# Kernel tuning notes

Hardware: AMD Instinct MI355X
Metric: run time of the kernel (lower is better)

Reference implementation:

```python
import math
import jax, jax.numpy as jnp
from jax import lax
import numpy as np

N = 512          # transform size; frame size = 2N
B = 16           # batch
T = 2048         # number of frames; signal length = N*T
PI = math.pi


def _make_mdct_filter(n: int, normalize: bool = True) -> jnp.ndarray:
    # filter[k, 0, t] = cos(pi/N * (t + 0.5 + N/2) * (k + 0.5)) / sqrt(N)
    k = jnp.arange(n, dtype=jnp.float32).reshape(n, 1, 1)
    t = jnp.arange(2 * n, dtype=jnp.float32).reshape(1, 1, 2 * n)
    f = jnp.cos(PI / n * (t + 0.5 + n / 2) * (k + 0.5))
    if normalize:
        f = f / jnp.sqrt(jnp.float32(n))
    return f  # [N, 1, 2N]


def setup_inputs() -> dict:
    key = jax.random.key(0)
    x = jax.random.normal(key, (B, 1, N * T), dtype=jnp.float32)
    mdct_filter = _make_mdct_filter(N, normalize=True)
    return {"x": x, "mdct_filter": mdct_filter}


def reference(x, mdct_filter):
    # Equivalent of F.conv1d(x, filter, stride=N, padding=N)
    n = mdct_filter.shape[0]
    # x: [B, 1, N*T] -> out: [B, N, T+1]
    out = lax.conv_general_dilated(
        x, mdct_filter,
        window_strides=(n,),
        padding=[(n, n)],
        dimension_numbers=("NCH", "OIH", "NCH"),
    )
    return out
```

## Files before the change

### kernel.cpp

```cpp
#include <hip/hip_runtime.h>
#include <hip/hip_bf16.h>
#include <stdint.h>
#include <stddef.h>


constexpr int N_ = 512;
constexpr int T_ = 2048;
constexpr int B_ = 16;
constexpr int LEN = N_ * T_;
constexpr int FRAMES = T_ + 1;
constexpr int COLS = B_ * FRAMES;
constexpr int NT_TILES = 257;
constexpr int COLS_PAD = NT_TILES * 128;
constexpr int KF = 512;
constexpr int BK = 64;

typedef __attribute__((ext_vector_type(8))) _Float16 f16x8;
typedef __attribute__((ext_vector_type(4))) _Float16 f16x4;
typedef __attribute__((ext_vector_type(4))) float f32x4;

#define GLD16(gptr, lptr)                                                     \
  __builtin_amdgcn_global_load_lds(                                           \
      (const __attribute__((address_space(1))) unsigned int*)(gptr),          \
      (__attribute__((address_space(3))) unsigned int*)(lptr), 16, 0, 0)

__global__ void prep_filter(const float* __restrict__ f,
                            _Float16* __restrict__ D) {
  int idx = (blockIdx.x * 256 + threadIdx.x) * 4;
  int k = idx >> 9;
  int j = idx & 511;
  int t = (j < 256) ? j : (j + 256);
  const float4 v = *(const float4*)&f[k * 1024 + t];
  f16x4 h = {(_Float16)v.x, (_Float16)v.y, (_Float16)v.z, (_Float16)v.w};
  *(f16x4*)&D[k * KF + j] = h;
}

__global__ void fold_x(const float* __restrict__ x, _Float16* __restrict__ V) {
  const int c = blockIdx.x * 4 + (threadIdx.x >> 6);
  const int l = threadIdx.x & 63;
  const bool mi = (l < 32);
  const int j0 = mi ? (l * 8) : (256 + (l - 32) * 8);
  const float sgn = mi ? -1.0f : 1.0f;
  float4 a0 = {0.f, 0.f, 0.f, 0.f}, a1 = {0.f, 0.f, 0.f, 0.f};
  float4 r0 = {0.f, 0.f, 0.f, 0.f}, r1 = {0.f, 0.f, 0.f, 0.f};
  if (c < COLS) {
    int b = (int)((unsigned)c / (unsigned)FRAMES);
    int o = c - b * FRAMES;
    const int lo = b * LEN;
    const int g = lo + o * N_ - N_;
    const int fb = g + (mi ? j0 : (j0 + 256));
    const int rb = g + (mi ? (504 - j0) : (1272 - j0));
    if ((unsigned)(fb - lo) <= (unsigned)(LEN - 8)) {
      a0 = *(const float4*)(x + fb);
      a1 = *(const float4*)(x + fb + 4);
    }
    if ((unsigned)(rb - lo) <= (unsigned)(LEN - 8)) {
      r0 = *(const float4*)(x + rb);
      r1 = *(const float4*)(x + rb + 4);
    }
  }
  f16x8 h;
  h[0] = (_Float16)__builtin_fmaf(sgn, r1.w, a0.x);
  h[1] = (_Float16)__builtin_fmaf(sgn, r1.z, a0.y);
  h[2] = (_Float16)__builtin_fmaf(sgn, r1.y, a0.z);
  h[3] = (_Float16)__builtin_fmaf(sgn, r1.x, a0.w);
  h[4] = (_Float16)__builtin_fmaf(sgn, r0.w, a1.x);
  h[5] = (_Float16)__builtin_fmaf(sgn, r0.z, a1.y);
  h[6] = (_Float16)__builtin_fmaf(sgn, r0.y, a1.z);
  h[7] = (_Float16)__builtin_fmaf(sgn, r0.x, a1.w);
  if (c < COLS_PAD) *(f16x8*)&V[(size_t)c * KF + j0] = h;
}

__global__ __launch_bounds__(256, 4) void gemm_fold(
    const _Float16* __restrict__ D, const _Float16* __restrict__ V,
    float* __restrict__ out) {
  __shared__ __align__(16) _Float16 As[128 * BK];
  __shared__ __align__(16) _Float16 Bs[128 * BK];

  const int id = blockIdx.x;
  const int xcd = id & 7;
  const int sb = id >> 3;
  const int nt = (sb >> 2) * 8 + xcd;
  if (nt >= NT_TILES) return;
  const int m0 = (sb & 3) * 128;
  const int n0 = nt * 128;

  const int tid = threadIdx.x;
  const int wid = tid >> 6;
  const int lane = tid & 63;
  const int quad = lane >> 4;
  const int l16 = lane & 15;
  const int mw = (wid >> 1) * 64;
  const int nw = (wid & 1) * 64;

  f32x4 acc[4][4];
#pragma unroll
  for (int i = 0; i < 4; ++i)
#pragma unroll
    for (int j = 0; j < 4; ++j) acc[i][j] = (f32x4){0.f, 0.f, 0.f, 0.f};

  for (int kt = 0; kt < KF / BK; ++kt) {
    const int kb = kt * BK;
    __syncthreads();
#pragma unroll
    for (int it = 0; it < 4; ++it) {
      const int S = it * 256 + tid;
      const int r = S >> 3;
      const int c = (S & 7) ^ (r & 7);
      const int goff = kb + c * 8;
      GLD16(D + (size_t)(m0 + r) * KF + goff, &As[S * 8]);
      GLD16(V + (size_t)(n0 + r) * KF + goff, &Bs[S * 8]);
    }
    __syncthreads();

#pragma unroll
    for (int ko = 0; ko < 2; ++ko) {
      f16x8 af[4], bf[4];
#pragma unroll
      for (int i = 0; i < 4; ++i) {
        int ra = mw + i * 16 + l16;
        int rb = nw + i * 16 + l16;
        int ca = ko * 4 + quad;
        af[i] = *(const f16x8*)&As[(ra * 8 + (ca ^ (ra & 7))) * 8];
        bf[i] = *(const f16x8*)&Bs[(rb * 8 + (ca ^ (rb & 7))) * 8];
      }
#pragma unroll
      for (int i = 0; i < 4; ++i)
#pragma unroll
        for (int j = 0; j < 4; ++j)
          acc[i][j] = __builtin_amdgcn_mfma_f32_16x16x32_f16(af[i], bf[j], acc[i][j], 0, 0, 0);
    }
  }

#pragma unroll
  for (int i = 0; i < 4; ++i) {
#pragma unroll
    for (int j = 0; j < 4; ++j) {
      int col = n0 + nw + j * 16 + l16;
      if (col < COLS) {
        int b = col / FRAMES;
        int o = col - b * FRAMES;
        int rowb = m0 + mw + i * 16 + quad * 4;
        float* op = out + (size_t)b * N_ * FRAMES + (size_t)rowb * FRAMES + o;
#pragma unroll
        for (int r = 0; r < 4; ++r) op[(size_t)r * FRAMES] = acc[i][j][r];
      }
    }
  }
}

__global__ void naive_conv(const float* __restrict__ x, const float* __restrict__ f,
                           float* __restrict__ out) {
  int col = blockIdx.x;
  int k = threadIdx.x;
  __shared__ float win[1024];
  int b = col / FRAMES;
  int o = col - b * FRAMES;
  const float* xb = x + (size_t)b * LEN;
  int g = o * N_ - N_;
  for (int t = threadIdx.x; t < 1024; t += 512) {
    int i = g + t;
    win[t] = (i >= 0 && i < LEN) ? xb[i] : 0.0f;
  }
  __syncthreads();
  float s = 0.0f;
  const float* fk = f + (size_t)k * 1024;
  for (int t = 0; t < 1024; ++t) s += win[t] * fk[t];
  out[(size_t)b * N_ * FRAMES + (size_t)k * FRAMES + o] = s;
}

extern "C" void kernel_launch(void* const* d_in, const int* in_sizes, int n_in,
                              void* d_out, int out_size, void* d_ws, size_t ws_size,
                              hipStream_t stream) {
  const float* x = (const float*)d_in[0];
  const float* f = (const float*)d_in[1];
  float* out = (float*)d_out;

  const size_t elems_D = (size_t)512 * 512;
  const size_t elems_V = (size_t)COLS_PAD * KF;
  const size_t need = (elems_D + elems_V) * sizeof(_Float16);

  if (ws_size < need) {
    naive_conv<<<COLS, 512, 0, stream>>>(x, f, out);
    return;
  }

  _Float16* D = (_Float16*)d_ws;
  _Float16* V = D + elems_D;

  prep_filter<<<256, 256, 0, stream>>>(f, D);
  fold_x<<<COLS_PAD / 4, 256, 0, stream>>>(x, V);
  gemm_fold<<<1056, 256, 0, stream>>>(D, V, out);
}
```

Measured before the change: 144.8 us.

## Double-buffer LDS tiles in GEMM with halved K-step to overlap loads

Splits the shared-memory A/B tiles into two buffers and halves the K-tile to 32. While the MFMAs run on the current buffer, the direct-to-LDS global loads for the next K-tile are issued into the other buffer, with the XOR swizzle adapted to the 4-chunk row layout. The goal is to hide global-load latency behind compute and drop one barrier per iteration, at the cost of twice as many K iterations. Overlap may be lost if the compiler inserts a full vmcnt wait before each barrier.

```diff
diff --git a/kernel.cpp b/kernel.cpp
--- a/kernel.cpp
+++ b/kernel.cpp
@@ -13,7 +13,8 @@
 constexpr int NT_TILES = 257;
 constexpr int COLS_PAD = NT_TILES * 128;
 constexpr int KF = 512;
-constexpr int BK = 64;
+constexpr int BK = 32;
+constexpr int KI = KF / BK;
 
 typedef __attribute__((ext_vector_type(8))) _Float16 f16x8;
 typedef __attribute__((ext_vector_type(4))) _Float16 f16x4;
@@ -74,8 +75,8 @@
 __global__ __launch_bounds__(256, 4) void gemm_fold(
     const _Float16* __restrict__ D, const _Float16* __restrict__ V,
     float* __restrict__ out) {
-  __shared__ __align__(16) _Float16 As[128 * BK];
-  __shared__ __align__(16) _Float16 Bs[128 * BK];
+  __shared__ __align__(16) _Float16 As[2][128 * BK];
+  __shared__ __align__(16) _Float16 Bs[2][128 * BK];
 
   const int id = blockIdx.x;
   const int xcd = id & 7;
@@ -93,43 +94,48 @@
   const int mw = (wid >> 1) * 64;
   const int nw = (wid & 1) * 64;
 
+  const _Float16* Dm = D + (size_t)m0 * KF;
+  const _Float16* Vn = V + (size_t)n0 * KF;
+
   f32x4 acc[4][4];
 #pragma unroll
   for (int i = 0; i < 4; ++i)
 #pragma unroll
     for (int j = 0; j < 4; ++j) acc[i][j] = (f32x4){0.f, 0.f, 0.f, 0.f};
 
-  for (int kt = 0; kt < KF / BK; ++kt) {
-    const int kb = kt * BK;
+  auto stage = [&](int kb, int buf) {
+#pragma unroll
+    for (int u = 0; u < 2; ++u) {
+      const int S = u * 256 + tid;
+      const int r = S >> 2;
+      const int c = (S & 3) ^ ((r >> 1) & 3);
+      const int goff = kb + c * 8;
+      GLD16(Dm + (size_t)r * KF + goff, &As[buf][S * 8]);
+      GLD16(Vn + (size_t)r * KF + goff, &Bs[buf][S * 8]);
+    }
+  };
+
+  stage(0, 0);
+
+  for (int kt = 0; kt < KI; ++kt) {
+    const int cur = kt & 1;
+    const int nxt = cur ^ 1;
     __syncthreads();
-#pragma unroll
-    for (int it = 0; it < 4; ++it) {
-      const int S = it * 256 + tid;
-      const int r = S >> 3;
-      const int c = (S & 7) ^ (r & 7);
-      const int goff = kb + c * 8;
-      GLD16(D + (size_t)(m0 + r) * KF + goff, &As[S * 8]);
-      GLD16(V + (size_t)(n0 + r) * KF + goff, &Bs[S * 8]);
-    }
-    __syncthreads();
-
-#pragma unroll
-    for (int ko = 0; ko < 2; ++ko) {
-      f16x8 af[4], bf[4];
-#pragma unroll
-      for (int i = 0; i < 4; ++i) {
-        int ra = mw + i * 16 + l16;
-        int rb = nw + i * 16 + l16;
-        int ca = ko * 4 + quad;
-        af[i] = *(const f16x8*)&As[(ra * 8 + (ca ^ (ra & 7))) * 8];
-        bf[i] = *(const f16x8*)&Bs[(rb * 8 + (ca ^ (rb & 7))) * 8];
-      }
-#pragma unroll
-      for (int i = 0; i < 4; ++i)
-#pragma unroll
-        for (int j = 0; j < 4; ++j)
-          acc[i][j] = __builtin_amdgcn_mfma_f32_16x16x32_f16(af[i], bf[j], acc[i][j], 0, 0, 0);
-    }
+    if (kt + 1 < KI) stage((kt + 1) * BK, nxt);
+
+    f16x8 af[4], bf[4];
+#pragma unroll
+    for (int i = 0; i < 4; ++i) {
+      const int ra = mw + i * 16 + l16;
+      const int rb = nw + i * 16 + l16;
+      af[i] = *(const f16x8*)&As[cur][(ra * 4 + (quad ^ ((ra >> 1) & 3))) * 8];
+      bf[i] = *(const f16x8*)&Bs[cur][(rb * 4 + (quad ^ ((rb >> 1) & 3))) * 8];
+    }
+#pragma unroll
+    for (int i = 0; i < 4; ++i)
+#pragma unroll
+      for (int j = 0; j < 4; ++j)
+        acc[i][j] = __builtin_amdgcn_mfma_f32_16x16x32_f16(af[i], bf[j], acc[i][j], 0, 0, 0);
   }
 
 #pragma unroll
```

After: 151.7 us. +4.7%, slower.
